# Optimization experiments

Measured on AMD Instinct MI355X. Metric: run time of the kernel, lower is better.

Reference implementation:

```python
import jax, jax.numpy as jnp
import numpy as np
import math

B, NQ, G = 512, 1, 1000
H, IN, E = 8, 256, 128
KD = E // H  # key/val dim per head = 16
C = 10.0

def setup_inputs() -> dict:
    key = jax.random.key(0)
    ks = jax.random.split(key, 10)
    inp = {
        'decoder_input': jax.random.normal(ks[0], (B, NQ, IN), jnp.float32),
        'K': jax.random.normal(ks[1], (H, B, G, KD), jnp.float32),
        'V': jax.random.normal(ks[2], (H, B, G, KD), jnp.float32),
        'V_output': jax.random.normal(ks[3], (B, G, E), jnp.float32),
        'mask': jax.random.randint(ks[4], (B, NQ, G), 0, 2, jnp.int32),
        # learned params (uniform(-stdv, stdv) init as in the torch module)
        'W_emb': jax.random.uniform(ks[5], (E, IN), jnp.float32, -1/math.sqrt(IN), 1/math.sqrt(IN)),
        'b_emb': jax.random.uniform(ks[6], (E,), jnp.float32, -1/math.sqrt(IN), 1/math.sqrt(IN)),
        'W_query': jax.random.uniform(ks[7], (H, E, KD), jnp.float32, -1/math.sqrt(KD), 1/math.sqrt(KD)),
        'W_out': jax.random.uniform(ks[8], (H, KD, E), jnp.float32, -1/math.sqrt(E), 1/math.sqrt(E)),
        'W_q': jax.random.uniform(ks[9], (1, E, E), jnp.float32, -1/math.sqrt(E), 1/math.sqrt(E)),
    }
    return inp

def reference(decoder_input, K, V, V_output, mask, W_emb, b_emb, W_query, W_out, W_q):
    # mask==0 means attention not allowed (negative adjacency after the == 0 flip)
    m = (mask == 0)[None]                                   # (1, B, NQ, G), broadcasts over heads
    emb = decoder_input @ W_emb.T + b_emb                   # (B, NQ, E)
    Q = jnp.einsum('bqi,hik->hbqk', emb, W_query)           # (H, B, NQ, KD)
    compat = jnp.einsum('hbqk,hbgk->hbqg', Q, K) / jnp.sqrt(jnp.float32(KD))
    compat = jnp.where(m, -jnp.inf, compat)
    attn = jax.nn.softmax(compat, axis=-1)
    attn = jnp.where(m, 0.0, attn)                          # zero masked entries post-softmax
    heads = jnp.einsum('hbqg,hbgk->hbqk', attn, V)          # (H, B, NQ, KD)
    context = jnp.einsum('hbqk,hke->bqe', heads, W_out)     # (B, NQ, E) multi-head out proj
    Q2 = jnp.einsum('bqe,ef->bqf', context, W_q[0])         # (B, NQ, E)
    z = jnp.einsum('bqf,bgf->bqg', Q2, V_output) / jnp.sqrt(jnp.float32(E))
    return C * jnp.tanh(z)                                  # (B, NQ, G), softmax_output=False
```

## Files before the change

### kernel.cpp

```cpp
#include <hip/hip_runtime.h>
#include <math.h>

#define GG   1000
#define HH   8
#define KDIM 16
#define EDIM 128
#define INDIM 256
#define BDIM 256

__global__ __launch_bounds__(BDIM) void decoder_kernel(
    const float* __restrict__ dIn,
    const float* __restrict__ K,
    const float* __restrict__ V,
    const float* __restrict__ Vout,
    const int*   __restrict__ mask,
    const float* __restrict__ Wemb,
    const float* __restrict__ bemb,
    const float* __restrict__ Wq,
    const float* __restrict__ Wout,
    const float* __restrict__ WQ2,
    float* __restrict__ out,
    int B)
{
    const int b = blockIdx.x;
    const int t = threadIdx.x;

    __shared__ __align__(16) float s_din[INDIM];
    __shared__ __align__(16) float s_emb[EDIM];
    __shared__ __align__(16) float s_q[HH][KDIM];
    __shared__ int   s_mask[GG];
    __shared__ float s_attn[HH][GG];
    __shared__ __align__(16) float s_hp[HH][8][KDIM];
    __shared__ float s_invsum[HH];
    __shared__ float s_heads[HH * KDIM];
    __shared__ float s_ctx[EDIM];
    __shared__ __align__(16) float s_q2[EDIM];

    s_din[t] = dIn[(size_t)b * INDIM + t];
    for (int g = t; g < GG; g += BDIM) s_mask[g] = mask[(size_t)b * GG + g];
    __syncthreads();

    if (t < EDIM) {
        float acc = bemb[t];
        const float* w = Wemb + (size_t)t * INDIM;
        #pragma unroll 4
        for (int i = 0; i < INDIM; i += 4) {
            float4 wv = *(const float4*)(w + i);
            acc += wv.x * s_din[i] + wv.y * s_din[i + 1] +
                   wv.z * s_din[i + 2] + wv.w * s_din[i + 3];
        }
        s_emb[t] = acc;
    }
    __syncthreads();

    if (t < HH * KDIM) {
        int h = t >> 4, k = t & 15;
        float acc = 0.f;
        const float* w = Wq + (size_t)h * EDIM * KDIM + k;
        #pragma unroll 8
        for (int e = 0; e < EDIM; ++e) acc += s_emb[e] * w[e * KDIM];
        s_q[h][k] = acc * 0.25f;
    }
    __syncthreads();

    for (int h = 0; h < HH; ++h) {
        const float* Kh = K + ((size_t)h * B + b) * (size_t)(GG * KDIM);
        float4 q0 = *(const float4*)&s_q[h][0];
        float4 q1 = *(const float4*)&s_q[h][4];
        float4 q2 = *(const float4*)&s_q[h][8];
        float4 q3 = *(const float4*)&s_q[h][12];
        for (int g = t; g < GG; g += BDIM) {
            float c = -1e30f;
            if (s_mask[g] != 0) {
                const float4* kp = (const float4*)(Kh + (size_t)g * KDIM);
                float4 k0 = kp[0], k1 = kp[1], k2 = kp[2], k3 = kp[3];
                c  = q0.x * k0.x + q0.y * k0.y + q0.z * k0.z + q0.w * k0.w;
                c += q1.x * k1.x + q1.y * k1.y + q1.z * k1.z + q1.w * k1.w;
                c += q2.x * k2.x + q2.y * k2.y + q2.z * k2.z + q2.w * k2.w;
                c += q3.x * k3.x + q3.y * k3.y + q3.z * k3.z + q3.w * k3.w;
            }
            s_attn[h][g] = c;
        }
    }
    __syncthreads();

    {
        int h = t >> 5;
        int lane = t & 31;
        float m = -1e30f;
        for (int g = lane; g < GG; g += 32) m = fmaxf(m, s_attn[h][g]);
        #pragma unroll
        for (int off = 16; off; off >>= 1) m = fmaxf(m, __shfl_xor(m, off, 32));
        float s = 0.f;
        for (int g = lane; g < GG; g += 32) {
            float e = __expf(s_attn[h][g] - m);
            s_attn[h][g] = e;
            s += e;
        }
        #pragma unroll
        for (int off = 16; off; off >>= 1) s += __shfl_xor(s, off, 32);
        if (lane == 0) s_invsum[h] = 1.f / s;
    }
    __syncthreads();

    {
        int h   = t >> 5;
        int sub = (t >> 2) & 7;
        int k4  = t & 3;
        const float* Vh = V + ((size_t)h * B + b) * (size_t)(GG * KDIM);
        float4 acc = make_float4(0.f, 0.f, 0.f, 0.f);
        for (int g = sub; g < GG; g += 8) {
            float a = s_attn[h][g];
            if (a != 0.f) {
                float4 v = *(const float4*)(Vh + (size_t)g * KDIM + k4 * 4);
                acc.x += a * v.x; acc.y += a * v.y;
                acc.z += a * v.z; acc.w += a * v.w;
            }
        }
        s_hp[h][sub][k4 * 4 + 0] = acc.x;
        s_hp[h][sub][k4 * 4 + 1] = acc.y;
        s_hp[h][sub][k4 * 4 + 2] = acc.z;
        s_hp[h][sub][k4 * 4 + 3] = acc.w;
    }
    __syncthreads();
    if (t < HH * KDIM) {
        int h = t >> 4, k = t & 15;
        float sum = 0.f;
        #pragma unroll
        for (int sub = 0; sub < 8; ++sub) sum += s_hp[h][sub][k];
        s_heads[t] = sum * s_invsum[h];
    }
    __syncthreads();

    if (t < EDIM) {
        float acc = 0.f;
        #pragma unroll 8
        for (int j = 0; j < HH * KDIM; ++j) acc += s_heads[j] * Wout[(size_t)j * EDIM + t];
        s_ctx[t] = acc;
    }
    __syncthreads();
    if (t < EDIM) {
        float acc = 0.f;
        #pragma unroll 8
        for (int e = 0; e < EDIM; ++e) acc += s_ctx[e] * WQ2[(size_t)e * EDIM + t];
        s_q2[t] = acc * 0.08838834764831845f;
    }
    __syncthreads();

    const float* Vo = Vout + (size_t)b * (size_t)(GG * EDIM);
    for (int g = t; g < GG; g += BDIM) {
        const float4* vp = (const float4*)(Vo + (size_t)g * EDIM);
        float acc = 0.f;
        #pragma unroll 8
        for (int j = 0; j < EDIM / 4; ++j) {
            float4 v = vp[j];
            float4 q = *(const float4*)&s_q2[j * 4];
            acc += v.x * q.x + v.y * q.y + v.z * q.z + v.w * q.w;
        }
        out[(size_t)b * GG + g] = 10.f * tanhf(acc);
    }
}

extern "C" void kernel_launch(void* const* d_in, const int* in_sizes, int n_in,
                              void* d_out, int out_size, void* d_ws, size_t ws_size,
                              hipStream_t stream) {
    const float* dIn  = (const float*)d_in[0];
    const float* K    = (const float*)d_in[1];
    const float* V    = (const float*)d_in[2];
    const float* Vout = (const float*)d_in[3];
    const int*   mask = (const int*)d_in[4];
    const float* Wemb = (const float*)d_in[5];
    const float* bemb = (const float*)d_in[6];
    const float* Wq   = (const float*)d_in[7];
    const float* Wout = (const float*)d_in[8];
    const float* WQ2  = (const float*)d_in[9];
    float* out = (float*)d_out;

    int B = in_sizes[0] / INDIM;
    decoder_kernel<<<dim3(B), dim3(BDIM), 0, stream>>>(
        dIn, K, V, Vout, mask, Wemb, bemb, Wq, Wout, WQ2, out, B);
}
```

Before: 691.8 us.

## Split fused decoder into three kernels parallelised over heads and output chunks

Replaces the single per-batch kernel with three launches: embedding/query projection per batch, attention per (head, batch) block, and output projection plus logits split into four chunks per batch. The per-batch kernel had only 512 blocks doing serial head loops, so this is meant to expose far more parallelism for the memory-bound K/V and V_output streams. The logit stage now uses one 32-lane group per row with coalesced float4 loads and a shuffle reduction instead of one thread reading a whole strided row. It adds workspace round-trips, two extra launches, and recomputes the Wout/WQ2 projections in each of the four chunk blocks.

```diff
diff --git a/kernel.cpp b/kernel.cpp
--- a/kernel.cpp
+++ b/kernel.cpp
@@ -1,141 +1,156 @@
 #include <hip/hip_runtime.h>
 #include <math.h>
 
-#define GG   1000
-#define HH   8
-#define KDIM 16
-#define EDIM 128
+#define GG    1000
+#define HH    8
+#define KDIM  16
+#define EDIM  128
 #define INDIM 256
-#define BDIM 256
-
-__global__ __launch_bounds__(BDIM) void decoder_kernel(
+
+__global__ __launch_bounds__(128) void k1_embq(
     const float* __restrict__ dIn,
-    const float* __restrict__ K,
-    const float* __restrict__ V,
-    const float* __restrict__ Vout,
-    const int*   __restrict__ mask,
     const float* __restrict__ Wemb,
     const float* __restrict__ bemb,
     const float* __restrict__ Wq,
+    float* __restrict__ qout,
+    int B)
+{
+    const int b = blockIdx.x, t = threadIdx.x;
+    __shared__ __align__(16) float s_din[INDIM];
+    __shared__ float s_emb[EDIM];
+
+    s_din[t]       = dIn[(size_t)b * INDIM + t];
+    s_din[t + 128] = dIn[(size_t)b * INDIM + t + 128];
+    __syncthreads();
+
+    float acc = bemb[t];
+    const float* w = Wemb + (size_t)t * INDIM;
+    #pragma unroll 4
+    for (int i = 0; i < INDIM; i += 4) {
+        float4 wv = *(const float4*)(w + i);
+        acc += wv.x * s_din[i] + wv.y * s_din[i + 1] +
+               wv.z * s_din[i + 2] + wv.w * s_din[i + 3];
+    }
+    s_emb[t] = acc;
+    __syncthreads();
+
+    const int h = t >> 4, k = t & 15;
+    float q = 0.f;
+    const float* wq = Wq + (size_t)h * EDIM * KDIM + k;
+    #pragma unroll 8
+    for (int e = 0; e < EDIM; ++e) q += s_emb[e] * wq[e * KDIM];
+    qout[(size_t)b * EDIM + t] = q * 0.25f;
+}
+
+__global__ __launch_bounds__(256) void k2_attn(
+    const float* __restrict__ K,
+    const float* __restrict__ V,
+    const int*   __restrict__ mask,
+    const float* __restrict__ qin,
+    float* __restrict__ headsout,
+    int B)
+{
+    const int bx = blockIdx.x;
+    const int b = bx % B, h = bx / B;
+    const int t = threadIdx.x;
+
+    __shared__ int   s_mask[GG];
+    __shared__ float s_attn[GG];
+    __shared__ __align__(16) float s_q[KDIM];
+    __shared__ float s_red[8];
+    __shared__ __align__(16) float s_hp[64][KDIM];
+    __shared__ float s_bmax, s_binv;
+
+    if (t < KDIM) s_q[t] = qin[(size_t)b * EDIM + h * KDIM + t];
+    for (int g = t; g < GG; g += 256) s_mask[g] = mask[(size_t)b * GG + g];
+    __syncthreads();
+
+    const float* Kh = K + ((size_t)h * B + b) * (size_t)(GG * KDIM);
+    float4 q0 = *(const float4*)&s_q[0];
+    float4 q1 = *(const float4*)&s_q[4];
+    float4 q2 = *(const float4*)&s_q[8];
+    float4 q3 = *(const float4*)&s_q[12];
+    float lmax = -1e30f;
+    for (int g = t; g < GG; g += 256) {
+        float c = -1e30f;
+        if (s_mask[g] != 0) {
+            const float4* kp = (const float4*)(Kh + (size_t)g * KDIM);
+            float4 k0 = kp[0], k1 = kp[1], k2 = kp[2], k3 = kp[3];
+            c  = q0.x * k0.x + q0.y * k0.y + q0.z * k0.z + q0.w * k0.w;
+            c += q1.x * k1.x + q1.y * k1.y + q1.z * k1.z + q1.w * k1.w;
+            c += q2.x * k2.x + q2.y * k2.y + q2.z * k2.z + q2.w * k2.w;
+            c += q3.x * k3.x + q3.y * k3.y + q3.z * k3.z + q3.w * k3.w;
+        }
+        s_attn[g] = c;
+        lmax = fmaxf(lmax, c);
+    }
+    #pragma unroll
+    for (int off = 32; off; off >>= 1) lmax = fmaxf(lmax, __shfl_xor(lmax, off));
+    const int wid = t >> 6;
+    if ((t & 63) == 0) s_red[wid] = lmax;
+    __syncthreads();
+    if (t == 0) s_bmax = fmaxf(fmaxf(s_red[0], s_red[1]), fmaxf(s_red[2], s_red[3]));
+    __syncthreads();
+    const float m = s_bmax;
+
+    float lsum = 0.f;
+    for (int g = t; g < GG; g += 256) {
+        float e = __expf(s_attn[g] - m);
+        s_attn[g] = e;
+        lsum += e;
+    }
+    #pragma unroll
+    for (int off = 32; off; off >>= 1) lsum += __shfl_xor(lsum, off);
+    if ((t & 63) == 0) s_red[4 + wid] = lsum;
+    __syncthreads();
+    if (t == 0) s_binv = 1.f / (s_red[4] + s_red[5] + s_red[6] + s_red[7]);
+    __syncthreads();
+
+    const int sub = t >> 2, k4 = t & 3;
+    const float* Vh = V + ((size_t)h * B + b) * (size_t)(GG * KDIM);
+    float4 acc = make_float4(0.f, 0.f, 0.f, 0.f);
+    for (int g = sub; g < GG; g += 64) {
+        float a = s_attn[g];
+        if (a != 0.f) {
+            float4 v = *(const float4*)(Vh + (size_t)g * KDIM + k4 * 4);
+            acc.x += a * v.x; acc.y += a * v.y;
+            acc.z += a * v.z; acc.w += a * v.w;
+        }
+    }
+    s_hp[sub][k4 * 4 + 0] = acc.x;
+    s_hp[sub][k4 * 4 + 1] = acc.y;
+    s_hp[sub][k4 * 4 + 2] = acc.z;
+    s_hp[sub][k4 * 4 + 3] = acc.w;
+    __syncthreads();
+    if (t < KDIM) {
+        float s = 0.f;
+        #pragma unroll
+        for (int i = 0; i < 64; ++i) s += s_hp[i][t];
+        headsout[(size_t)b * EDIM + h * KDIM + t] = s * s_binv;
+    }
+}
+
+__global__ __launch_bounds__(256) void k3_out(
+    const float* __restrict__ Vout,
+    const float* __restrict__ headsin,
     const float* __restrict__ Wout,
     const float* __restrict__ WQ2,
     float* __restrict__ out,
     int B)
 {
-    const int b = blockIdx.x;
+    const int bx = blockIdx.x;
+    const int b = bx >> 2, chunk = bx & 3;
     const int t = threadIdx.x;
-
-    __shared__ __align__(16) float s_din[INDIM];
-    __shared__ __align__(16) float s_emb[EDIM];
-    __shared__ __align__(16) float s_q[HH][KDIM];
-    __shared__ int   s_mask[GG];
-    __shared__ float s_attn[HH][GG];
-    __shared__ __align__(16) float s_hp[HH][8][KDIM];
-    __shared__ float s_invsum[HH];
-    __shared__ float s_heads[HH * KDIM];
+    __shared__ float s_heads[EDIM];
     __shared__ float s_ctx[EDIM];
     __shared__ __align__(16) float s_q2[EDIM];
 
-    s_din[t] = dIn[(size_t)b * INDIM + t];
-    for (int g = t; g < GG; g += BDIM) s_mask[g] = mask[(size_t)b * GG + g];
-    __syncthreads();
-
-    if (t < EDIM) {
-        float acc = bemb[t];
-        const float* w = Wemb + (size_t)t * INDIM;
-        #pragma unroll 4
-        for (int i = 0; i < INDIM; i += 4) {
-            float4 wv = *(const float4*)(w + i);
-            acc += wv.x * s_din[i] + wv.y * s_din[i + 1] +
-                   wv.z * s_din[i + 2] + wv.w * s_din[i + 3];
-        }
-        s_emb[t] = acc;
-    }
-    __syncthreads();
-
-    if (t < HH * KDIM) {
-        int h = t >> 4, k = t & 15;
-        float acc = 0.f;
-        const float* w = Wq + (size_t)h * EDIM * KDIM + k;
-        #pragma unroll 8
-        for (int e = 0; e < EDIM; ++e) acc += s_emb[e] * w[e * KDIM];
-        s_q[h][k] = acc * 0.25f;
-    }
-    __syncthreads();
-
-    for (int h = 0; h < HH; ++h) {
-        const float* Kh = K + ((size_t)h * B + b) * (size_t)(GG * KDIM);
-        float4 q0 = *(const float4*)&s_q[h][0];
-        float4 q1 = *(const float4*)&s_q[h][4];
-        float4 q2 = *(const float4*)&s_q[h][8];
-        float4 q3 = *(const float4*)&s_q[h][12];
-        for (int g = t; g < GG; g += BDIM) {
-            float c = -1e30f;
-            if (s_mask[g] != 0) {
-                const float4* kp = (const float4*)(Kh + (size_t)g * KDIM);
-                float4 k0 = kp[0], k1 = kp[1], k2 = kp[2], k3 = kp[3];
-                c  = q0.x * k0.x + q0.y * k0.y + q0.z * k0.z + q0.w * k0.w;
-                c += q1.x * k1.x + q1.y * k1.y + q1.z * k1.z + q1.w * k1.w;
-                c += q2.x * k2.x + q2.y * k2.y + q2.z * k2.z + q2.w * k2.w;
-                c += q3.x * k3.x + q3.y * k3.y + q3.z * k3.z + q3.w * k3.w;
-            }
-            s_attn[h][g] = c;
-        }
-    }
-    __syncthreads();
-
-    {
-        int h = t >> 5;
-        int lane = t & 31;
-        float m = -1e30f;
-        for (int g = lane; g < GG; g += 32) m = fmaxf(m, s_attn[h][g]);
-        #pragma unroll
-        for (int off = 16; off; off >>= 1) m = fmaxf(m, __shfl_xor(m, off, 32));
-        float s = 0.f;
-        for (int g = lane; g < GG; g += 32) {
-            float e = __expf(s_attn[h][g] - m);
-            s_attn[h][g] = e;
-            s += e;
-        }
-        #pragma unroll
-        for (int off = 16; off; off >>= 1) s += __shfl_xor(s, off, 32);
-        if (lane == 0) s_invsum[h] = 1.f / s;
-    }
-    __syncthreads();
-
-    {
-        int h   = t >> 5;
-        int sub = (t >> 2) & 7;
-        int k4  = t & 3;
-        const float* Vh = V + ((size_t)h * B + b) * (size_t)(GG * KDIM);
-        float4 acc = make_float4(0.f, 0.f, 0.f, 0.f);
-        for (int g = sub; g < GG; g += 8) {
-            float a = s_attn[h][g];
-            if (a != 0.f) {
-                float4 v = *(const float4*)(Vh + (size_t)g * KDIM + k4 * 4);
-                acc.x += a * v.x; acc.y += a * v.y;
-                acc.z += a * v.z; acc.w += a * v.w;
-            }
-        }
-        s_hp[h][sub][k4 * 4 + 0] = acc.x;
-        s_hp[h][sub][k4 * 4 + 1] = acc.y;
-        s_hp[h][sub][k4 * 4 + 2] = acc.z;
-        s_hp[h][sub][k4 * 4 + 3] = acc.w;
-    }
-    __syncthreads();
-    if (t < HH * KDIM) {
-        int h = t >> 4, k = t & 15;
-        float sum = 0.f;
-        #pragma unroll
-        for (int sub = 0; sub < 8; ++sub) sum += s_hp[h][sub][k];
-        s_heads[t] = sum * s_invsum[h];
-    }
-    __syncthreads();
-
+    if (t < EDIM) s_heads[t] = headsin[(size_t)b * EDIM + t];
+    __syncthreads();
     if (t < EDIM) {
         float acc = 0.f;
         #pragma unroll 8
-        for (int j = 0; j < HH * KDIM; ++j) acc += s_heads[j] * Wout[(size_t)j * EDIM + t];
+        for (int j = 0; j < EDIM; ++j) acc += s_heads[j] * Wout[(size_t)j * EDIM + t];
         s_ctx[t] = acc;
     }
     __syncthreads();
@@ -147,17 +162,19 @@
     }
     __syncthreads();
 
+    const int lane = t & 31;
+    const int rowoff = t >> 5;
+    float4 q = *(const float4*)&s_q2[lane * 4];
     const float* Vo = Vout + (size_t)b * (size_t)(GG * EDIM);
-    for (int g = t; g < GG; g += BDIM) {
+    const int g0 = chunk * (GG / 4);
+    const int g1 = g0 + (GG / 4);
+    for (int g = g0 + rowoff; g < g1; g += 8) {
         const float4* vp = (const float4*)(Vo + (size_t)g * EDIM);
-        float acc = 0.f;
-        #pragma unroll 8
-        for (int j = 0; j < EDIM / 4; ++j) {
-            float4 v = vp[j];
-            float4 q = *(const float4*)&s_q2[j * 4];
-            acc += v.x * q.x + v.y * q.y + v.z * q.z + v.w * q.w;
-        }
-        out[(size_t)b * GG + g] = 10.f * tanhf(acc);
+        float4 v = vp[lane];
+        float acc = v.x * q.x + v.y * q.y + v.z * q.z + v.w * q.w;
+        #pragma unroll
+        for (int off = 16; off; off >>= 1) acc += __shfl_xor(acc, off, 32);
+        if (lane == 0) out[(size_t)b * GG + g] = 10.f * tanhf(acc);
     }
 }
 
@@ -176,7 +193,11 @@
     const float* WQ2  = (const float*)d_in[9];
     float* out = (float*)d_out;
 
-    int B = in_sizes[0] / INDIM;
-    decoder_kernel<<<dim3(B), dim3(BDIM), 0, stream>>>(
-        dIn, K, V, Vout, mask, Wemb, bemb, Wq, Wout, WQ2, out, B);
-}
+    const int B = in_sizes[0] / INDIM;
+    float* ws_q     = (float*)d_ws;
+    float* ws_heads = ws_q + (size_t)B * EDIM;
+
+    k1_embq<<<dim3(B), dim3(128), 0, stream>>>(dIn, Wemb, bemb, Wq, ws_q, B);
+    k2_attn<<<dim3(HH * B), dim3(256), 0, stream>>>(K, V, mask, ws_q, ws_heads, B);
+    k3_out<<<dim3(B * 4), dim3(256), 0, stream>>>(Vout, ws_heads, Wout, WQ2, out, B);
+}
```

Result: faster. 677.1 us (-2.1%).
